# Performance work log

Measured on AMD Instinct MI355X. Metric: run time of the kernel, lower is better.

Reference implementation:

```python
import jax, jax.numpy as jnp
import numpy as np

B, M, C, D, FF, FEAT = 1, 1024, 128, 512, 1024, 20
PAIR = 3 * D + 2 * FEAT  # slow_scorer_size = 1576


def _ffnn(x, W0, b0, W1, b1):
    # FFNN(depth=1): hidden relu layer then linear output (eval mode, no dropout)
    return jax.nn.relu(x @ W0 + b0) @ W1 + b1


def _batch_gather(x, idx):
    # x: [B, M, ...], idx: [B, ...] int -> gather along mention dim per batch
    return jax.vmap(lambda xb, ib: xb[ib])(x, idx)


def _bucket_distance(d):
    # log-scale distance buckets 0..9 (identity for d<=4)
    log_idx = jnp.floor(jnp.log(jnp.maximum(d, 1).astype(jnp.float32)) / jnp.log(2.0)).astype(jnp.int32) + 3
    return jnp.clip(jnp.where(d <= 4, d, log_idx), 0, 9)


def setup_inputs() -> dict:
    key = jax.random.key(0)
    ks = jax.random.split(key, 10)
    s = 0.02
    return {
        'mention_emb': jax.random.normal(ks[0], (B, M, D), dtype=jnp.float32),
        'mention_cluster_ids': jax.random.randint(ks[1], (B, M), 0, 200),
        'mention_speaker_ids': jax.random.randint(ks[2], (B, M), 0, 2),
        'ms_W0': jax.random.normal(ks[3], (D, FF), dtype=jnp.float32) * s,
        'ms_b0': jnp.zeros((FF,), jnp.float32),
        'ms_W1': jax.random.normal(ks[4], (FF, 1), dtype=jnp.float32) * s,
        'ms_b1': jnp.zeros((1,), jnp.float32),
        'sp_W0': jax.random.normal(ks[5], (PAIR, FF), dtype=jnp.float32) * s,
        'sp_b0': jnp.zeros((FF,), jnp.float32),
        'sp_W1': jax.random.normal(ks[6], (FF, 1), dtype=jnp.float32) * s,
        'sp_b1': jnp.zeros((1,), jnp.float32),
        'speaker_emb': jax.random.normal(ks[7], (2, FEAT), dtype=jnp.float32) * s,
        'bucket_emb': jax.random.normal(ks[8], (10, FEAT), dtype=jnp.float32) * s,
    }


def reference(mention_emb, mention_cluster_ids, mention_speaker_ids,
              ms_W0, ms_b0, ms_W1, ms_b1,
              sp_W0, sp_b0, sp_W1, sp_b1,
              speaker_emb, bucket_emb):
    # mention scoring
    mention_scores = _ffnn(mention_emb, ms_W0, ms_b0, ms_W1, ms_b1)[..., 0]  # [B, M]

    # get_antecedent_info: fixed window of C previous mentions
    offsets = jnp.arange(1, C + 1)[None, None, :]                    # [1,1,C]
    raw = jnp.arange(M)[None, :, None] - offsets                      # [1,M,C]
    antecedents = jnp.broadcast_to(jnp.clip(raw, 0, M - 1), (B, M, C))
    ant_mask = jnp.broadcast_to(raw >= 0, (B, M, C))

    fast_scores = _batch_gather(mention_scores, antecedents) + mention_scores[:, :, None]
    antecedent_emb = _batch_gather(mention_emb, antecedents)          # [B,M,C,D]

    # slow pair scorer features
    same_speaker = (_batch_gather(mention_speaker_ids, antecedents) == mention_speaker_ids[:, :, None]).astype(jnp.int32)
    speaker_feat = speaker_emb[same_speaker]                          # [B,M,C,FEAT]
    bucket_feat = jnp.broadcast_to(bucket_emb[_bucket_distance(offsets)], (B, M, C, FEAT))

    src = jnp.broadcast_to(mention_emb[:, :, None, :], (B, M, C, D))
    pair_emb = jnp.concatenate([src, antecedent_emb, src * antecedent_emb, speaker_feat, bucket_feat], axis=-1)
    slow_scores = _ffnn(pair_emb, sp_W0, sp_b0, sp_W1, sp_b1)[..., 0]  # [B,M,C]

    antecedent_scores = fast_scores + slow_scores + jnp.log(ant_mask.astype(jnp.float32))
    overall_scores = jnp.concatenate([jnp.zeros((B, M, 1), jnp.float32), antecedent_scores], axis=2)
    overall_dist = jax.nn.softmax(overall_scores, axis=-1)
    eps = 1e-6
    overall_dist = jnp.clip(overall_dist, eps, 1.0 - eps)
    overall_dist = overall_dist / jnp.sum(overall_dist, axis=-1, keepdims=True)

    # coref loss from cluster ids
    ant_cluster = _batch_gather(mention_cluster_ids, antecedents) * ant_mask.astype(mention_cluster_ids.dtype)
    same_cluster = ant_cluster == mention_cluster_ids[:, :, None]
    non_dummy = (mention_cluster_ids > 0)[:, :, None]
    ant_labels = same_cluster & non_dummy
    dummy_labels = ~jnp.any(ant_labels, axis=2, keepdims=True)
    overall_labels = jnp.concatenate([dummy_labels, ant_labels], axis=2)
    loss = -jnp.sum(jnp.log(overall_dist) * overall_labels.astype(jnp.float32), axis=2)
    loss = jnp.mean(jnp.sum(loss, axis=1))
    return overall_dist, loss
```

## Files before the change

kernel.cpp:

```cpp
#include <hip/hip_runtime.h>
#include <math.h>

#define MM 1024
#define DD 512
#define CC 128
#define LDSR 516


typedef __attribute__((ext_vector_type(8))) short bf16x8;
typedef __attribute__((ext_vector_type(4), aligned(8))) short bf16x4a;
typedef __attribute__((ext_vector_type(4))) float f32x4;

__device__ __forceinline__ ushort bf16_rn(float x) {
    uint u = __float_as_uint(x);
    uint r = u + 0x7fffu + ((u >> 16) & 1u);
    return (ushort)(r >> 16);
}
__device__ __forceinline__ float bf16_to_f(ushort u) {
    return __uint_as_float(((uint)u) << 16);
}
__device__ __forceinline__ bf16x8 ld_lds16(const ushort* p) {
    bf16x4a lo = *(const bf16x4a*)p;
    bf16x4a hi = *(const bf16x4a*)(p + 4);
    return __builtin_shufflevector(lo, hi, 0, 1, 2, 3, 4, 5, 6, 7);
}

__global__ __launch_bounds__(256) void prep_all(
    const float* __restrict__ emb, ushort* __restrict__ embb,
    const float* __restrict__ ms_W0, const float* __restrict__ sp_W0,
    ushort* __restrict__ Wall, ushort* __restrict__ WfragP,
    const float* __restrict__ speaker_emb, const float* __restrict__ bucket_emb,
    float* __restrict__ spk_proj, float* __restrict__ bkt_proj)
{
    const int bid = blockIdx.x;
    const int tid = threadIdx.x;

    if (bid < 1024) {
        int i = bid * 256 + tid;
        float2 v = ((const float2*)emb)[i];
        ushort2 o;
        o.x = bf16_rn(v.x);
        o.y = bf16_rn(v.y);
        ((ushort2*)embb)[i] = o;
        return;
    }
    if (bid < 1408) {
        __shared__ float t[64][65];
        const int r = bid - 1024;
        const int k0 = (r & 7) * 64;
        const int n0 = (r >> 3) * 64;
        const int g = n0 >> 10;
        const float* src = (g == 0) ? ms_W0 : (sp_W0 + (size_t)(g - 1) * 512 * 1024);
        const int col0 = n0 & 1023;
        const int tr = tid >> 6, tc = tid & 63;
#pragma unroll
        for (int i = 0; i < 16; ++i) {
            int k = tr + i * 4;
            t[k][tc] = src[(size_t)(k0 + k) * 1024 + col0 + tc];
        }
        __syncthreads();
        const int f = tid >> 2;
        const int c4 = tid & 3;
        ushort tmp[16];
#pragma unroll
        for (int j = 0; j < 16; ++j) tmp[j] = bf16_rn(t[c4 * 16 + j][f]);
        uint4* dst = (uint4*)(Wall + (size_t)(n0 + f) * 512 + k0 + c4 * 16);
        dst[0] = *(uint4*)&tmp[0];
        dst[1] = *(uint4*)&tmp[8];
        return;
    }
    if (bid < 1664) {
        const int b4 = (bid - 1408) * 4 + (tid >> 6);
        const int l = tid & 63;
        const int g2 = b4 >> 5, s = (b4 >> 1) & 15, j = b4 & 1;
        const int wv = g2 >> 2, ft = g2 & 3;
        const int t16 = wv * 8 + ft * 2 + j;
        const int f = t16 * 16 + (l & 15);
        const int kb = s * 32 + ((l >> 4) & 3) * 8;
        const float* W = sp_W0 + (size_t)1024 * 1024;
        ushort tmp[8];
#pragma unroll
        for (int e = 0; e < 8; ++e) tmp[e] = bf16_rn(W[(size_t)(kb + e) * 1024 + f]);
        uint4* dst = (uint4*)(WfragP + (size_t)b4 * 512 + l * 8);
        *dst = *(uint4*)&tmp[0];
        return;
    }
    {
        const int r = bid - 1664;
        const float* e; const float* W; float* out;
        if (r < 2) { e = speaker_emb + r * 20; W = sp_W0 + (size_t)1536 * 1024; out = spk_proj + r * 1024; }
        else       { e = bucket_emb + (r - 2) * 20; W = sp_W0 + (size_t)1556 * 1024; out = bkt_proj + (r - 2) * 1024; }
        float ek[20];
#pragma unroll
        for (int k = 0; k < 20; ++k) ek[k] = e[k];
        for (int f = tid; f < 1024; f += 256) {
            float s = 0.f;
#pragma unroll
            for (int k = 0; k < 20; ++k) s = fmaf(ek[k], W[(size_t)k * 1024 + f], s);
            out[f] = s;
        }
        return;
    }
}

__global__ __launch_bounds__(256) void gemm_h_ms(
    const ushort* __restrict__ embb, const ushort* __restrict__ Wall,
    const float* __restrict__ ms_b0, const float* __restrict__ ms_W1,
    float* __restrict__ H, float* __restrict__ ms)
{
    const int n0 = blockIdx.x * 128;
    const int m0 = blockIdx.y * 128;
    const int lane = threadIdx.x & 63, wave = threadIdx.x >> 6;
    const int wx = wave & 1, wy = wave >> 1;
    const int l15 = lane & 15, lq = lane >> 4;

    const ushort* arow[4];
#pragma unroll
    for (int mi = 0; mi < 4; ++mi)
        arow[mi] = embb + (size_t)(m0 + wy * 64 + mi * 16 + l15) * 512;
    const ushort* brow[4];
#pragma unroll
    for (int ni = 0; ni < 4; ++ni)
        brow[ni] = Wall + (size_t)(n0 + wx * 64 + ni * 16 + l15) * 512;

    f32x4 acc[4][4];
#pragma unroll
    for (int i = 0; i < 4; ++i)
#pragma unroll
        for (int j = 0; j < 4; ++j) acc[i][j] = (f32x4)0.f;

    for (int kt = 0; kt < 512; kt += 32) {
        const int ko = kt + lq * 8;
        bf16x8 av[4], bv[4];
#pragma unroll
        for (int mi = 0; mi < 4; ++mi) av[mi] = *(const bf16x8*)(arow[mi] + ko);
#pragma unroll
        for (int ni = 0; ni < 4; ++ni) bv[ni] = *(const bf16x8*)(brow[ni] + ko);
#pragma unroll
        for (int mi = 0; mi < 4; ++mi)
#pragma unroll
            for (int ni = 0; ni < 4; ++ni)
                acc[mi][ni] = __builtin_amdgcn_mfma_f32_16x16x32_bf16(av[mi], bv[ni], acc[mi][ni], 0, 0, 0);
    }

    if (n0 < 1024) {
        float b0v[4], w1v[4];
#pragma unroll
        for (int ni = 0; ni < 4; ++ni) {
            const int col = n0 + wx * 64 + ni * 16 + l15;
            b0v[ni] = ms_b0[col];
            w1v[ni] = ms_W1[col];
        }
#pragma unroll
        for (int mi = 0; mi < 4; ++mi)
#pragma unroll
            for (int r = 0; r < 4; ++r) {
                float s = 0.f;
#pragma unroll
                for (int ni = 0; ni < 4; ++ni)
                    s += fmaxf(acc[mi][ni][r] + b0v[ni], 0.f) * w1v[ni];
                s += __shfl_xor(s, 1); s += __shfl_xor(s, 2);
                s += __shfl_xor(s, 4); s += __shfl_xor(s, 8);
                if (l15 == 0) {
                    const int mrow = m0 + wy * 64 + mi * 16 + lq * 4 + r;
                    atomicAdd(&ms[mrow], s);
                }
            }
    } else {
#pragma unroll
        for (int mi = 0; mi < 4; ++mi)
#pragma unroll
            for (int r = 0; r < 4; ++r) {
                int mrow = m0 + wy * 64 + mi * 16 + lq * 4 + r;
#pragma unroll
                for (int ni = 0; ni < 4; ++ni)
                    H[(size_t)mrow * 3072 + n0 + wx * 64 + ni * 16 + l15] = acc[mi][ni][r];
            }
    }
}

__global__ __launch_bounds__(512, 8) void pair_mfma(
    const ushort* __restrict__ embb, const ushort* __restrict__ WfragP,
    const float* __restrict__ H, const float* __restrict__ spk_proj,
    const float* __restrict__ bkt_proj, const float* __restrict__ sp_b0,
    const float* __restrict__ sp_W1, const int* __restrict__ speaker,
    float* __restrict__ slow)
{
    extern __shared__ ushort Alds[];
    float* red = (float*)(Alds + 32 * LDSR);
    int* meta_ss = (int*)(red + 8 * 32);
    int* meta_bk = meta_ss + 32;
    const int m = blockIdx.x;
    const int cq = blockIdx.y;
    const int cbase = cq * 32;
    const int tid = threadIdx.x;
    const int spk_m = speaker[m];

    {
        const int c = tid & 31;
        const int kh = (tid >> 5) * 32;
        int a = m - 1 - (cbase + c); if (a < 0) a = 0;
        const ushort* ea = embb + (size_t)a * 512 + kh;
        const ushort* em = embb + (size_t)m * 512 + kh;
        ushort* dst = Alds + c * LDSR + kh;
#pragma unroll
        for (int j = 0; j < 32; j += 8) {
            bf16x8 va = *(const bf16x8*)(ea + j);
            bf16x8 vm = *(const bf16x8*)(em + j);
            uint pr[4];
#pragma unroll
            for (int p = 0; p < 4; ++p) {
                float q0 = bf16_to_f((ushort)va[2 * p])     * bf16_to_f((ushort)vm[2 * p]);
                float q1 = bf16_to_f((ushort)va[2 * p + 1]) * bf16_to_f((ushort)vm[2 * p + 1]);
                pr[p] = __builtin_amdgcn_perm(__float_as_uint(q1), __float_as_uint(q0), 0x07060302u);
            }
            *(uint2*)(dst + j)     = *(uint2*)&pr[0];
            *(uint2*)(dst + j + 4) = *(uint2*)&pr[2];
        }
        if (tid < 32) {
            meta_ss[c] = (speaker[a] == spk_m) ? 1 : 0;
            int off = cbase + c + 1;
            int bk;
            if (off <= 4) bk = off;
            else { bk = 31 - __clz(off) + 3; if (bk > 9) bk = 9; }
            meta_bk[c] = bk;
        }
    }
    __syncthreads();

    const int lane = tid & 63;
    const int wave = __builtin_amdgcn_readfirstlane(tid >> 6);
    const int l15 = lane & 15, lq = lane >> 4;
    const ushort* ab0 = Alds + l15 * LDSR + lq * 8;

    const float* Hsrc = H + m * 3072 + 1024;
    const float* Hant = H + 2048;

    float sacc[2][4];
#pragma unroll
    for (int ct = 0; ct < 2; ++ct)
#pragma unroll
        for (int r = 0; r < 4; ++r) sacc[ct][r] = 0.f;

#pragma unroll 1
    for (int ft = 0; ft < 4; ++ft) {
        const int f0a = wave * 128 + ft * 32;
        const ushort* bb = WfragP + (size_t)(wave * 4 + ft) * 16384 + (size_t)lane * 8;
        f32x4 acc[2][2];
#pragma unroll
        for (int i = 0; i < 2; ++i)
#pragma unroll
            for (int j = 0; j < 2; ++j) acc[i][j] = (f32x4)0.f;

#pragma unroll 4
        for (int s = 0; s < 16; ++s) {
            bf16x8 b0 = *(const bf16x8*)(bb + s * 1024);
            bf16x8 b1 = *(const bf16x8*)(bb + s * 1024 + 512);
            bf16x8 a0 = ld_lds16(ab0 + s * 32);
            bf16x8 a1 = ld_lds16(ab0 + 16 * LDSR + s * 32);
            __builtin_amdgcn_s_setprio(1);
            acc[0][0] = __builtin_amdgcn_mfma_f32_16x16x32_bf16(a0, b0, acc[0][0], 0, 0, 0);
            acc[0][1] = __builtin_amdgcn_mfma_f32_16x16x32_bf16(a0, b1, acc[0][1], 0, 0, 0);
            acc[1][0] = __builtin_amdgcn_mfma_f32_16x16x32_bf16(a1, b0, acc[1][0], 0, 0, 0);
            acc[1][1] = __builtin_amdgcn_mfma_f32_16x16x32_bf16(a1, b1, acc[1][1], 0, 0, 0);
            __builtin_amdgcn_s_setprio(0);
        }

        float srcb[2], w1v[2], sp0v[2], sp1v[2];
#pragma unroll
        for (int fi = 0; fi < 2; ++fi) {
            const int fcol = f0a + fi * 16 + l15;
            srcb[fi] = Hsrc[fcol] + sp_b0[fcol];
            w1v[fi]  = sp_W1[fcol];
            sp0v[fi] = spk_proj[fcol];
            sp1v[fi] = spk_proj[1024 + fcol];
        }
#pragma unroll
        for (int ct = 0; ct < 2; ++ct) {
#pragma unroll
            for (int reg = 0; reg < 4; ++reg) {
                const int cl = ct * 16 + lq * 4 + reg;
                int a = m - 1 - (cbase + cl); if (a < 0) a = 0;
                const int ss = meta_ss[cl];
                const int aidx = a * 3072;
                const int bidx = meta_bk[cl] << 10;
                float s = sacc[ct][reg];
#pragma unroll
                for (int fi = 0; fi < 2; ++fi) {
                    const int fcol = f0a + fi * 16 + l15;
                    float bval = bkt_proj[bidx + fcol];
                    float pre = acc[ct][fi][reg] + srcb[fi] + Hant[aidx + fcol]
                              + (ss ? sp1v[fi] : sp0v[fi]) + bval;
                    s += fmaxf(pre, 0.f) * w1v[fi];
                }
                sacc[ct][reg] = s;
            }
        }
    }

#pragma unroll
    for (int ct = 0; ct < 2; ++ct) {
#pragma unroll
        for (int reg = 0; reg < 4; ++reg) {
            float s = sacc[ct][reg];
            s += __shfl_xor(s, 1); s += __shfl_xor(s, 2);
            s += __shfl_xor(s, 4); s += __shfl_xor(s, 8);
            if (l15 == 0) red[wave * 32 + ct * 16 + lq * 4 + reg] = s;
        }
    }
    __syncthreads();
    if (tid < 32) {
        float s = 0.f;
#pragma unroll
        for (int i = 0; i < 8; ++i) s += red[i * 32 + tid];
        slow[m * 128 + cbase + tid] = s;
    }
}

__device__ __forceinline__ float bsum2(float v, float* sm) {
#pragma unroll
    for (int o = 1; o < 64; o <<= 1) v += __shfl_xor(v, o);
    __syncthreads();
    if ((threadIdx.x & 63) == 0) sm[threadIdx.x >> 6] = v;
    __syncthreads();
    return sm[0] + sm[1];
}
__device__ __forceinline__ float bmax2(float v, float* sm) {
#pragma unroll
    for (int o = 1; o < 64; o <<= 1) v = fmaxf(v, __shfl_xor(v, o));
    __syncthreads();
    if ((threadIdx.x & 63) == 0) sm[threadIdx.x >> 6] = v;
    __syncthreads();
    return fmaxf(sm[0], sm[1]);
}

__global__ __launch_bounds__(128) void softmax_loss(
    const float* __restrict__ slow, const float* __restrict__ ms,
    const float* __restrict__ ms_b1,
    const float* __restrict__ sp_b1, const int* __restrict__ cluster,
    float* __restrict__ out, float* __restrict__ loss_partial)
{
    const int m = blockIdx.x, c = threadIdx.x;
    __shared__ float sm[2];
    const int raw = m - 1 - c;
    const bool maskv = raw >= 0;
    const int a = maskv ? raw : 0;
    float score = slow[(size_t)m * 128 + c] + sp_b1[0]
                + ms[m] + ms[a] + 2.f * ms_b1[0];
    if (!maskv) score = -INFINITY;

    float mx = fmaxf(bmax2(score, sm), 0.f);
    float e = expf(score - mx);
    float e0 = expf(0.f - mx);
    float sum = bsum2(e, sm) + e0;
    float p = e / sum, p0 = e0 / sum;
    const float eps = 1e-6f;
    p  = fminf(fmaxf(p,  eps), 1.f - eps);
    p0 = fminf(fmaxf(p0, eps), 1.f - eps);
    float sum2 = bsum2(p, sm) + p0;
    p /= sum2; p0 /= sum2;
    out[(size_t)m * 129 + 1 + c] = p;
    if (c == 0) out[(size_t)m * 129] = p0;

    const int cid = cluster[m];
    const bool lbl = maskv && (cid > 0) && (cluster[a] == cid);
    float anyc = bsum2(lbl ? 1.f : 0.f, sm);
    float lsum = bsum2(lbl ? -logf(p) : 0.f, sm);
    if (c == 0) {
        if (anyc == 0.f) lsum += -logf(p0);
        loss_partial[m] = lsum;
    }
}

__global__ void loss_sum(const float* __restrict__ lp, float* __restrict__ out) {
    float v = 0.f;
    for (int i = threadIdx.x; i < 1024; i += 256) v += lp[i];
#pragma unroll
    for (int o = 1; o < 64; o <<= 1) v += __shfl_xor(v, o);
    __shared__ float sm[4];
    if ((threadIdx.x & 63) == 0) sm[threadIdx.x >> 6] = v;
    __syncthreads();
    if (threadIdx.x == 0) out[(size_t)1024 * 129] = sm[0] + sm[1] + sm[2] + sm[3];
}

extern "C" void kernel_launch(void* const* d_in, const int* in_sizes, int n_in,
                              void* d_out, int out_size, void* d_ws, size_t ws_size,
                              hipStream_t stream)
{
    const float* emb   = (const float*)d_in[0];
    const int*   clus  = (const int*)  d_in[1];
    const int*   spk   = (const int*)  d_in[2];
    const float* ms_W0 = (const float*)d_in[3];
    const float* ms_b0 = (const float*)d_in[4];
    const float* ms_W1 = (const float*)d_in[5];
    const float* ms_b1 = (const float*)d_in[6];
    const float* sp_W0 = (const float*)d_in[7];
    const float* sp_b0 = (const float*)d_in[8];
    const float* sp_W1 = (const float*)d_in[9];
    const float* sp_b1 = (const float*)d_in[10];
    const float* spke  = (const float*)d_in[11];
    const float* bkte  = (const float*)d_in[12];

    float* ws = (float*)d_ws;
    float* H        = ws;
    float* slow     = ws + 3145728;
    float* spk_proj = ws + 3276800;
    float* bkt_proj = ws + 3278848;
    float* msc      = ws + 3289088;
    float* lossp    = ws + 3290112;
    ushort* embb    = (ushort*)(ws + 3291136);
    ushort* Wall    = (ushort*)(ws + 3553280);
    ushort* WfragP  = Wall + (size_t)3072 * 512;
    float* out = (float*)d_out;

    const int pair_lds = 32 * LDSR * 2 + 8 * 32 * 4 + 2 * 32 * 4;

    static bool attr_set = false;
    if (!attr_set) {
        hipFuncSetAttribute((const void*)&pair_mfma,
                            hipFuncAttributeMaxDynamicSharedMemorySize,
                            pair_lds);
        attr_set = true;
    }

    hipMemsetAsync(msc, 0, 1024 * sizeof(float), stream);
    hipLaunchKernelGGL(prep_all, dim3(1676), dim3(256), 0, stream,
                       emb, embb, ms_W0, sp_W0, Wall, WfragP,
                       spke, bkte, spk_proj, bkt_proj);
    hipLaunchKernelGGL(gemm_h_ms, dim3(24, 8), dim3(256), 0, stream,
                       embb, Wall, ms_b0, ms_W1, H, msc);
    hipLaunchKernelGGL(pair_mfma, dim3(1024, 4), dim3(512), pair_lds, stream,
                       embb, WfragP, H, spk_proj, bkt_proj, sp_b0, sp_W1, spk, slow);
    hipLaunchKernelGGL(softmax_loss, dim3(1024), dim3(128), 0, stream,
                       slow, msc, ms_b1, sp_b1, clus, out, lossp);
    hipLaunchKernelGGL(loss_sum, dim3(1), dim3(256), 0, stream, lossp, out);
}
```

Before: 329.2 us.

## Fold memset into prep, shrink GEMM tiles, precompute pair epilogue metadata

Drops the separate hipMemsetAsync by zeroing the mention-score accumulator inside the prep kernel. Shrinks gemm_h_ms tiles from 128x128 to 64x64, giving 768 blocks instead of 192 so more CUs are used, at the cost of less register reuse and more atomics. In pair_mfma it precomputes antecedent row offsets and bucket offsets in LDS and folds the source+bias term into the speaker projections, which cuts per-element adds in the epilogue.

```diff
diff --git a/kernel.cpp b/kernel.cpp
--- a/kernel.cpp
+++ b/kernel.cpp
@@ -30,7 +30,8 @@
     const float* __restrict__ ms_W0, const float* __restrict__ sp_W0,
     ushort* __restrict__ Wall, ushort* __restrict__ WfragP,
     const float* __restrict__ speaker_emb, const float* __restrict__ bucket_emb,
-    float* __restrict__ spk_proj, float* __restrict__ bkt_proj)
+    float* __restrict__ spk_proj, float* __restrict__ bkt_proj,
+    float* __restrict__ msc)
 {
     const int bid = blockIdx.x;
     const int tid = threadIdx.x;
@@ -87,6 +88,9 @@
     }
     {
         const int r = bid - 1664;
+        if (r == 0) {
+            for (int i = tid; i < 1024; i += 256) msc[i] = 0.f;
+        }
         const float* e; const float* W; float* out;
         if (r < 2) { e = speaker_emb + r * 20; W = sp_W0 + (size_t)1536 * 1024; out = spk_proj + r * 1024; }
         else       { e = bucket_emb + (r - 2) * 20; W = sp_W0 + (size_t)1556 * 1024; out = bkt_proj + (r - 2) * 1024; }
@@ -108,73 +112,73 @@
     const float* __restrict__ ms_b0, const float* __restrict__ ms_W1,
     float* __restrict__ H, float* __restrict__ ms)
 {
-    const int n0 = blockIdx.x * 128;
-    const int m0 = blockIdx.y * 128;
+    const int n0 = blockIdx.x * 64;
+    const int m0 = blockIdx.y * 64;
     const int lane = threadIdx.x & 63, wave = threadIdx.x >> 6;
     const int wx = wave & 1, wy = wave >> 1;
     const int l15 = lane & 15, lq = lane >> 4;
 
-    const ushort* arow[4];
-#pragma unroll
-    for (int mi = 0; mi < 4; ++mi)
-        arow[mi] = embb + (size_t)(m0 + wy * 64 + mi * 16 + l15) * 512;
-    const ushort* brow[4];
-#pragma unroll
-    for (int ni = 0; ni < 4; ++ni)
-        brow[ni] = Wall + (size_t)(n0 + wx * 64 + ni * 16 + l15) * 512;
-
-    f32x4 acc[4][4];
-#pragma unroll
-    for (int i = 0; i < 4; ++i)
-#pragma unroll
-        for (int j = 0; j < 4; ++j) acc[i][j] = (f32x4)0.f;
+    const ushort* arow[2];
+#pragma unroll
+    for (int mi = 0; mi < 2; ++mi)
+        arow[mi] = embb + (size_t)(m0 + wy * 32 + mi * 16 + l15) * 512;
+    const ushort* brow[2];
+#pragma unroll
+    for (int ni = 0; ni < 2; ++ni)
+        brow[ni] = Wall + (size_t)(n0 + wx * 32 + ni * 16 + l15) * 512;
+
+    f32x4 acc[2][2];
+#pragma unroll
+    for (int i = 0; i < 2; ++i)
+#pragma unroll
+        for (int j = 0; j < 2; ++j) acc[i][j] = (f32x4)0.f;
 
     for (int kt = 0; kt < 512; kt += 32) {
         const int ko = kt + lq * 8;
-        bf16x8 av[4], bv[4];
-#pragma unroll
-        for (int mi = 0; mi < 4; ++mi) av[mi] = *(const bf16x8*)(arow[mi] + ko);
-#pragma unroll
-        for (int ni = 0; ni < 4; ++ni) bv[ni] = *(const bf16x8*)(brow[ni] + ko);
-#pragma unroll
-        for (int mi = 0; mi < 4; ++mi)
-#pragma unroll
-            for (int ni = 0; ni < 4; ++ni)
+        bf16x8 av[2], bv[2];
+#pragma unroll
+        for (int mi = 0; mi < 2; ++mi) av[mi] = *(const bf16x8*)(arow[mi] + ko);
+#pragma unroll
+        for (int ni = 0; ni < 2; ++ni) bv[ni] = *(const bf16x8*)(brow[ni] + ko);
+#pragma unroll
+        for (int mi = 0; mi < 2; ++mi)
+#pragma unroll
+            for (int ni = 0; ni < 2; ++ni)
                 acc[mi][ni] = __builtin_amdgcn_mfma_f32_16x16x32_bf16(av[mi], bv[ni], acc[mi][ni], 0, 0, 0);
     }
 
     if (n0 < 1024) {
-        float b0v[4], w1v[4];
-#pragma unroll
-        for (int ni = 0; ni < 4; ++ni) {
-            const int col = n0 + wx * 64 + ni * 16 + l15;
+        float b0v[2], w1v[2];
+#pragma unroll
+        for (int ni = 0; ni < 2; ++ni) {
+            const int col = n0 + wx * 32 + ni * 16 + l15;
             b0v[ni] = ms_b0[col];
             w1v[ni] = ms_W1[col];
         }
 #pragma unroll
-        for (int mi = 0; mi < 4; ++mi)
+        for (int mi = 0; mi < 2; ++mi)
 #pragma unroll
             for (int r = 0; r < 4; ++r) {
                 float s = 0.f;
 #pragma unroll
-                for (int ni = 0; ni < 4; ++ni)
+                for (int ni = 0; ni < 2; ++ni)
                     s += fmaxf(acc[mi][ni][r] + b0v[ni], 0.f) * w1v[ni];
                 s += __shfl_xor(s, 1); s += __shfl_xor(s, 2);
                 s += __shfl_xor(s, 4); s += __shfl_xor(s, 8);
                 if (l15 == 0) {
-                    const int mrow = m0 + wy * 64 + mi * 16 + lq * 4 + r;
+                    const int mrow = m0 + wy * 32 + mi * 16 + lq * 4 + r;
                     atomicAdd(&ms[mrow], s);
                 }
             }
     } else {
 #pragma unroll
-        for (int mi = 0; mi < 4; ++mi)
+        for (int mi = 0; mi < 2; ++mi)
 #pragma unroll
             for (int r = 0; r < 4; ++r) {
-                int mrow = m0 + wy * 64 + mi * 16 + lq * 4 + r;
-#pragma unroll
-                for (int ni = 0; ni < 4; ++ni)
-                    H[(size_t)mrow * 3072 + n0 + wx * 64 + ni * 16 + l15] = acc[mi][ni][r];
+                int mrow = m0 + wy * 32 + mi * 16 + lq * 4 + r;
+#pragma unroll
+                for (int ni = 0; ni < 2; ++ni)
+                    H[(size_t)mrow * 3072 + n0 + wx * 32 + ni * 16 + l15] = acc[mi][ni][r];
             }
     }
 }
@@ -188,8 +192,9 @@
 {
     extern __shared__ ushort Alds[];
     float* red = (float*)(Alds + 32 * LDSR);
-    int* meta_ss = (int*)(red + 8 * 32);
-    int* meta_bk = meta_ss + 32;
+    int* meta_ai = (int*)(red + 8 * 32);
+    int* meta_sb = meta_ai + 32;
+    int* meta_bi = meta_sb + 32;
     const int m = blockIdx.x;
     const int cq = blockIdx.y;
     const int cbase = cq * 32;
@@ -218,12 +223,13 @@
             *(uint2*)(dst + j + 4) = *(uint2*)&pr[2];
         }
         if (tid < 32) {
-            meta_ss[c] = (speaker[a] == spk_m) ? 1 : 0;
+            meta_sb[c] = (speaker[a] == spk_m) ? 1 : 0;
+            meta_ai[c] = a * 3072;
             int off = cbase + c + 1;
             int bk;
             if (off <= 4) bk = off;
             else { bk = 31 - __clz(off) + 3; if (bk > 9) bk = 9; }
-            meta_bk[c] = bk;
+            meta_bi[c] = bk << 10;
         }
     }
     __syncthreads();
@@ -266,31 +272,29 @@
             __builtin_amdgcn_s_setprio(0);
         }
 
-        float srcb[2], w1v[2], sp0v[2], sp1v[2];
+        float w1v[2], sp0v[2], sp1v[2];
 #pragma unroll
         for (int fi = 0; fi < 2; ++fi) {
             const int fcol = f0a + fi * 16 + l15;
-            srcb[fi] = Hsrc[fcol] + sp_b0[fcol];
+            const float srcb = Hsrc[fcol] + sp_b0[fcol];
             w1v[fi]  = sp_W1[fcol];
-            sp0v[fi] = spk_proj[fcol];
-            sp1v[fi] = spk_proj[1024 + fcol];
+            sp0v[fi] = spk_proj[fcol] + srcb;
+            sp1v[fi] = spk_proj[1024 + fcol] + srcb;
         }
 #pragma unroll
         for (int ct = 0; ct < 2; ++ct) {
 #pragma unroll
             for (int reg = 0; reg < 4; ++reg) {
                 const int cl = ct * 16 + lq * 4 + reg;
-                int a = m - 1 - (cbase + cl); if (a < 0) a = 0;
-                const int ss = meta_ss[cl];
-                const int aidx = a * 3072;
-                const int bidx = meta_bk[cl] << 10;
+                const int ss = meta_sb[cl];
+                const int aidx = meta_ai[cl];
+                const int bidx = meta_bi[cl];
                 float s = sacc[ct][reg];
 #pragma unroll
                 for (int fi = 0; fi < 2; ++fi) {
                     const int fcol = f0a + fi * 16 + l15;
-                    float bval = bkt_proj[bidx + fcol];
-                    float pre = acc[ct][fi][reg] + srcb[fi] + Hant[aidx + fcol]
-                              + (ss ? sp1v[fi] : sp0v[fi]) + bval;
+                    float pre = acc[ct][fi][reg] + (ss ? sp1v[fi] : sp0v[fi])
+                              + Hant[aidx + fcol] + bkt_proj[bidx + fcol];
                     s += fmaxf(pre, 0.f) * w1v[fi];
                 }
                 sacc[ct][reg] = s;
@@ -413,7 +417,7 @@
     ushort* WfragP  = Wall + (size_t)3072 * 512;
     float* out = (float*)d_out;
 
-    const int pair_lds = 32 * LDSR * 2 + 8 * 32 * 4 + 2 * 32 * 4;
+    const int pair_lds = 32 * LDSR * 2 + 8 * 32 * 4 + 3 * 32 * 4;
 
     static bool attr_set = false;
     if (!attr_set) {
@@ -423,11 +427,10 @@
         attr_set = true;
     }
 
-    hipMemsetAsync(msc, 0, 1024 * sizeof(float), stream);
     hipLaunchKernelGGL(prep_all, dim3(1676), dim3(256), 0, stream,
                        emb, embb, ms_W0, sp_W0, Wall, WfragP,
-                       spke, bkte, spk_proj, bkt_proj);
-    hipLaunchKernelGGL(gemm_h_ms, dim3(24, 8), dim3(256), 0, stream,
+                       spke, bkte, spk_proj, bkt_proj, msc);
+    hipLaunchKernelGGL(gemm_h_ms, dim3(48, 16), dim3(256), 0, stream,
                        embb, Wall, ms_b0, ms_W1, H, msc);
     hipLaunchKernelGGL(pair_mfma, dim3(1024, 4), dim3(512), pair_lds, stream,
                        embb, WfragP, H, spk_proj, bkt_proj, sp_b0, sp_W1, spk, slow);
```

Result: no change. 329.6 us, median of 3 (+0.1%).
